# Kernel optimization log

Measured on AMD Instinct MI355X. Metric: run time of the kernel, lower is better.

Reference implementation:

```python
import jax, jax.numpy as jnp
import numpy as np

THRESHOLD = 0.5
SLACK = 3
EPS = 1e-12
B, H, W = 16, 512, 512


def _shift(p, dy, dx, b, h, w):
    # p is zero-padded by 1 on spatial dims; returns neighbor at offset (dy, dx)
    return p[:, 1 + dy:1 + dy + h, 1 + dx:1 + dx + w]


def _thin_sub(img, step):
    # One Zhang-Suen sub-iteration on bool image [B,H,W] (zero boundary, as skimage)
    b, h, w = img.shape
    p = jnp.pad(img.astype(jnp.int32), ((0, 0), (1, 1), (1, 1)))
    # P2..P9 clockwise starting at North
    P2 = _shift(p, -1, 0, b, h, w); P3 = _shift(p, -1, 1, b, h, w)
    P4 = _shift(p, 0, 1, b, h, w);  P5 = _shift(p, 1, 1, b, h, w)
    P6 = _shift(p, 1, 0, b, h, w);  P7 = _shift(p, 1, -1, b, h, w)
    P8 = _shift(p, 0, -1, b, h, w); P9 = _shift(p, -1, -1, b, h, w)
    seq = [P2, P3, P4, P5, P6, P7, P8, P9, P2]
    Bn = P2 + P3 + P4 + P5 + P6 + P7 + P8 + P9          # neighbor count
    A = sum((1 - seq[k]) * seq[k + 1] for k in range(8))  # 0->1 transitions
    cond = (Bn >= 2) & (Bn <= 6) & (A == 1)
    if step == 0:
        cond = cond & (P2 * P4 * P6 == 0) & (P4 * P6 * P8 == 0)
    else:
        cond = cond & (P2 * P4 * P8 == 0) & (P2 * P6 * P8 == 0)
    return img & ~cond


def _skeletonize(img):
    # Iterate Zhang-Suen thinning to convergence (skimage.morphology.skeletonize 2D = Zhang's method)
    def body(state):
        cur, _ = state
        nxt = _thin_sub(_thin_sub(cur, 0), 1)
        return (nxt, jnp.any(nxt != cur))

    out, _ = jax.lax.while_loop(lambda s: s[1], body, (img, jnp.array(True)))
    return out


def _edt_sq(mask):
    # Exact squared Euclidean distance to nearest True pixel, separable 2-pass.
    b, h, w = mask.shape
    BIG = h + w  # larger than any attainable 1D distance
    g = jnp.where(mask, 0, BIG).astype(jnp.int32)  # [B,H,W]

    # pass 1: 1D nearest-True distance along rows (axis=1) via fwd/bwd scans
    def fscan(carry, row):
        d = jnp.minimum(row, carry + 1)
        return d, d

    g_rows = jnp.moveaxis(g, 1, 0)  # [H,B,W]
    init = jnp.full((b, w), BIG, jnp.int32)
    _, fwd = jax.lax.scan(fscan, init, g_rows)
    _, bwd = jax.lax.scan(fscan, init, g_rows[::-1])
    f = jnp.minimum(jnp.minimum(fwd, bwd[::-1]), BIG)  # [H,B,W]
    f2 = jnp.moveaxis(f * f, 0, 1)  # [B,H,W] squared vertical distance

    # pass 2: d2[b,i,j] = min_{j'} f2[b,i,j'] + (j-j')^2 (lower envelope, memory-friendly lax.map)
    js = jnp.arange(w, dtype=jnp.int32)

    def one_col(j):
        off = (js - j) ** 2  # [W]
        return jnp.min(f2 + off[None, None, :], axis=-1)  # [B,H]

    d2 = jax.lax.map(one_col, js)  # [W,B,H]
    return jnp.transpose(d2, (1, 2, 0))  # [B,H,W]


def setup_inputs() -> dict:
    key = jax.random.key(0)
    k1, k2 = jax.random.split(key)
    y_pred = jax.random.uniform(k1, (B, H, W), dtype=jnp.float32)
    y_true = jax.random.uniform(k2, (B, H, W), dtype=jnp.float32)
    return {"y_pred": y_pred, "y_true": y_true}


def reference(y_pred, y_true):
    p = y_pred > THRESHOLD  # greater_is_road=True binarization
    g = y_true > THRESHOLD
    p = _skeletonize(p)
    g = _skeletonize(g)
    d2_gt = _edt_sq(g)   # EDT of ~g == distance to nearest g pixel
    d2_pr = _edt_sq(p)
    s2 = SLACK * SLACK   # dist <= slack  <=>  dist^2 <= slack^2 (integer sq EDT)
    tp_area = d2_gt <= s2
    fp_area = ~tp_area
    fn_area = d2_pr > s2
    ax = (1, 2)
    TP = jnp.sum(tp_area & p, ax).astype(jnp.float32)
    FP = jnp.sum(fp_area & p, ax).astype(jnp.float32)
    FN = jnp.sum(fn_area & g, ax).astype(jnp.float32)
    correctness = TP / (TP + FP + EPS)
    completeness = TP / (TP + FN + EPS)
    quality = TP / (TP + FP + FN + EPS)
    # mean over batch -> [3]: [correctness, completeness, quality]
    return jnp.mean(jnp.stack([correctness, completeness, quality], axis=1), axis=0)
```

## Files before the change

kernel.cpp:

```cpp
#include <hip/hip_runtime.h>
#include <stdint.h>

#define HH 512
#define WW 512
#define WPR 8
#define NWORDS (HH * WPR)
#define NTHREADS 1024
#define WPT (NWORDS / NTHREADS)
#define NB 16

typedef unsigned long long u64;

__device__ __forceinline__ u64 ldw(const u64* M, int r, int c) {
    return (r < 0 || r >= HH || c < 0 || c >= WPR) ? 0ULL : M[r * WPR + c];
}

__device__ __forceinline__ u64 zs_word(const u64* M, int r, int c, int step) {
    u64 nm = ldw(M, r - 1, c - 1), nc = ldw(M, r - 1, c), np = ldw(M, r - 1, c + 1);
    u64 cm = ldw(M, r,     c - 1), cc = ldw(M, r,     c), cp = ldw(M, r,     c + 1);
    u64 sm = ldw(M, r + 1, c - 1), sc = ldw(M, r + 1, c), sp = ldw(M, r + 1, c + 1);

    u64 P2 = nc;
    u64 P3 = (nc >> 1) | (np << 63);
    u64 P4 = (cc >> 1) | (cp << 63);
    u64 P5 = (sc >> 1) | (sp << 63);
    u64 P6 = sc;
    u64 P7 = (sc << 1) | (sm >> 63);
    u64 P8 = (cc << 1) | (cm >> 63);
    u64 P9 = (nc << 1) | (nm >> 63);

    u64 ab = P2 ^ P3;
    u64 s1 = ab ^ P4, c1 = (P2 & P3) | (ab & P4);
    u64 de = P5 ^ P6;
    u64 s2 = de ^ P7, c2 = (P5 & P6) | (de & P7);
    u64 s3 = P8 ^ P9, c3 = P8 & P9;
    u64 gh = s1 ^ s2;
    u64 b0 = gh ^ s3, c4 = (s1 & s2) | (gh & s3);
    u64 ij = c1 ^ c2;
    u64 s4 = ij ^ c3, c5 = (c1 & c2) | (ij & c3);
    u64 b1 = s4 ^ c4, c6 = s4 & c4;
    u64 b2 = c5 ^ c6, b3 = c5 & c6;

    u64 Bge2 = b1 | b2 | b3;
    u64 Ble6 = ~(b3 | (b2 & b1 & b0));

    u64 a1, a2, t;
    t = ~P2 & P3; a1 = t; a2 = 0ULL;
    t = ~P3 & P4; a2 |= a1 & t; a1 |= t;
    t = ~P4 & P5; a2 |= a1 & t; a1 |= t;
    t = ~P5 & P6; a2 |= a1 & t; a1 |= t;
    t = ~P6 & P7; a2 |= a1 & t; a1 |= t;
    t = ~P7 & P8; a2 |= a1 & t; a1 |= t;
    t = ~P8 & P9; a2 |= a1 & t; a1 |= t;
    t = ~P9 & P2; a2 |= a1 & t; a1 |= t;
    u64 Aeq1 = a1 & ~a2;

    u64 sccond;
    if (step == 0) sccond = ~(P2 & P4 & P6) & ~(P4 & P6 & P8);
    else           sccond = ~(P2 & P4 & P8) & ~(P2 & P6 & P8);

    return cc & ~(Bge2 & Ble6 & Aeq1 & sccond);
}

__global__ __launch_bounds__(NTHREADS)
void skel_kernel(const float* __restrict__ y_pred,
                 const float* __restrict__ y_true,
                 u64* __restrict__ skel ,
                 int* __restrict__ cnt ) {
    __shared__ u64 M[NWORDS];
    __shared__ unsigned int Cp[HH + 2];
    __shared__ int s_any[2];

    int bx = blockIdx.x;
    int tid = threadIdx.x;
    int lane = tid & 63;

    if (bx == 0 && tid < 4 * NB) cnt[tid] = 0;

    const float* src = (bx < NB) ? y_pred + (size_t)bx * HH * WW
                                 : y_true + (size_t)(bx - NB) * HH * WW;

    {
        unsigned short* M16 = (unsigned short*)M;
        const float4* s4 = (const float4*)src;
        #pragma unroll
        for (int i = 0; i < 16; ++i) {
            int t = i * NTHREADS + tid;
            float4 a = s4[t * 4 + 0];
            float4 b = s4[t * 4 + 1];
            float4 c = s4[t * 4 + 2];
            float4 d = s4[t * 4 + 3];
            unsigned bits =
                ((unsigned)(a.x > 0.5f) << 0)  | ((unsigned)(a.y > 0.5f) << 1)  |
                ((unsigned)(a.z > 0.5f) << 2)  | ((unsigned)(a.w > 0.5f) << 3)  |
                ((unsigned)(b.x > 0.5f) << 4)  | ((unsigned)(b.y > 0.5f) << 5)  |
                ((unsigned)(b.z > 0.5f) << 6)  | ((unsigned)(b.w > 0.5f) << 7)  |
                ((unsigned)(c.x > 0.5f) << 8)  | ((unsigned)(c.y > 0.5f) << 9)  |
                ((unsigned)(c.z > 0.5f) << 10) | ((unsigned)(c.w > 0.5f) << 11) |
                ((unsigned)(d.x > 0.5f) << 12) | ((unsigned)(d.y > 0.5f) << 13) |
                ((unsigned)(d.z > 0.5f) << 14) | ((unsigned)(d.w > 0.5f) << 15);
            M16[t] = (unsigned short)bits;
        }
    }

    for (int i = tid; i < HH + 2; i += NTHREADS)
        Cp[i] = (i >= 1 && i <= HH) ? 0x1FEu : 0u;
    if (tid < 2) s_any[tid] = 0;

    unsigned dl[WPT];
    #pragma unroll
    for (int k = 0; k < WPT; ++k) dl[k] = 0x1FEu;

    int p = 0;
    for (;;) {
        for (int step = 0; step < 2; ++step) {
            __syncthreads();
            u64 nv[WPT];
            u64 bal[WPT];
            bool anyc = false;
            #pragma unroll
            for (int k = 0; k < WPT; ++k) {
                int wi = k * NTHREADS + tid;
                int r = wi >> 3, c = wi & 7;
                unsigned need = ((Cp[r] | Cp[r + 1] | Cp[r + 2]) >> c) & 7u;
                bool chg = false;
                u64 x = 0;
                if (need) {
                    u64 cur = M[wi];
                    x = zs_word(M, r, c, step);
                    chg = (x != cur);
                }
                nv[k] = x;
                bal[k] = __ballot(chg);
                anyc |= (bal[k] != 0);
            }
            __syncthreads();
            #pragma unroll
            for (int k = 0; k < WPT; ++k) {
                int wi = k * NTHREADS + tid;
                if ((bal[k] >> lane) & 1) M[wi] = nv[k];
                if ((lane & 7) == 0) {
                    unsigned byte = ((unsigned)(bal[k] >> lane) & 0xFFu) << 1;
                    int idx = (wi >> 3) + 1;
                    Cp[idx] = byte | dl[k];
                    dl[k] = byte;
                }
            }
            if (anyc) s_any[p] = 1;
        }
        __syncthreads();
        int done = (s_any[p] == 0);
        if (tid == 0) s_any[p ^ 1] = 0;
        p ^= 1;
        if (done) break;
    }

    u64* dst = skel + (size_t)bx * NWORDS;
    #pragma unroll
    for (int k = 0; k < WPT; ++k) {
        int wi = k * NTHREADS + tid;
        dst[wi] = M[wi];
    }
}

#define STRIPS 8
#define SROWS (HH / STRIPS)
#define SR2 (SROWS + 6)

__device__ __forceinline__ u64 ldws(const u64* M, int r, int c) {
    return (c < 0 || c >= WPR) ? 0ULL : M[r * WPR + c];
}

__device__ __forceinline__ u64 dil3s(const u64* M, int r, int c) {
    u64 cm = ldws(M, r, c - 1), cc = ldws(M, r, c), cp = ldws(M, r, c + 1);
    u64 h = cc
          | (cc >> 1) | (cp << 63)
          | (cc >> 2) | (cp << 62)
          | (cc >> 3) | (cp << 61)
          | (cc << 1) | (cm >> 63)
          | (cc << 2) | (cm >> 62)
          | (cc << 3) | (cm >> 61);
    u64 um = ldws(M, r - 1, c - 1) | ldws(M, r + 1, c - 1) | ldws(M, r - 2, c - 1) | ldws(M, r + 2, c - 1);
    u64 uc = ldws(M, r - 1, c    ) | ldws(M, r + 1, c    ) | ldws(M, r - 2, c    ) | ldws(M, r + 2, c    );
    u64 up = ldws(M, r - 1, c + 1) | ldws(M, r + 1, c + 1) | ldws(M, r - 2, c + 1) | ldws(M, r + 2, c + 1);
    h |= uc
       | (uc >> 1) | (up << 63)
       | (uc >> 2) | (up << 62)
       | (uc << 1) | (um >> 63)
       | (uc << 2) | (um >> 62);
    h |= ldws(M, r - 3, c) | ldws(M, r + 3, c);
    return h;
}

__global__ __launch_bounds__(256)
void count_kernel(const u64* __restrict__ skel, int* __restrict__ cnt) {
    __shared__ u64 P[SR2 * WPR];
    __shared__ u64 G[SR2 * WPR];
    __shared__ int acc[4];

    int b = blockIdx.x / STRIPS;
    int s = blockIdx.x % STRIPS;
    int tid = threadIdx.x;
    int r0 = s * SROWS - 3;

    const u64* sp = skel + (size_t)b * NWORDS;
    const u64* sg = skel + (size_t)(NB + b) * NWORDS;
    for (int i = tid; i < SR2 * WPR; i += 256) {
        int gr = r0 + (i >> 3);
        bool in = (gr >= 0 && gr < HH);
        int gi = gr * WPR + (i & 7);
        P[i] = in ? sp[gi] : 0ULL;
        G[i] = in ? sg[gi] : 0ULL;
    }
    if (tid < 4) acc[tid] = 0;
    __syncthreads();

    int cp = 0, cg = 0, tp = 0, fnh = 0;
    #pragma unroll
    for (int k = 0; k < 2; ++k) {
        int w = k * 256 + tid;
        int r = (w >> 3) + 3, c = w & 7;
        u64 pw = P[r * WPR + c], gw = G[r * WPR + c];
        cp  += __popcll(pw);
        cg  += __popcll(gw);
        tp  += __popcll(pw & dil3s(G, r, c));
        fnh += __popcll(gw & dil3s(P, r, c));
    }
    #pragma unroll
    for (int o = 32; o > 0; o >>= 1) {
        cp  += __shfl_down(cp, o);
        cg  += __shfl_down(cg, o);
        tp  += __shfl_down(tp, o);
        fnh += __shfl_down(fnh, o);
    }
    if ((tid & 63) == 0) {
        atomicAdd(&acc[0], cp);
        atomicAdd(&acc[1], cg);
        atomicAdd(&acc[2], tp);
        atomicAdd(&acc[3], fnh);
    }
    __syncthreads();
    if (tid < 4) atomicAdd(&cnt[b * 4 + tid], acc[tid]);
}

__global__ void ccq_reduce(const int* __restrict__ cnt, float* __restrict__ out) {
    int k = threadIdx.x;
    if (k < 3) {
        float s = 0.0f;
        for (int b = 0; b < NB; ++b) {
            float TP = (float)cnt[b * 4 + 2];
            float FP = (float)(cnt[b * 4 + 0] - cnt[b * 4 + 2]);
            float FN = (float)(cnt[b * 4 + 1] - cnt[b * 4 + 3]);
            float v = (k == 0) ? TP / (TP + FP + 1e-12f)
                    : (k == 1) ? TP / (TP + FN + 1e-12f)
                               : TP / (TP + FP + FN + 1e-12f);
            s += v;
        }
        out[k] = s * (1.0f / NB);
    }
}

extern "C" void kernel_launch(void* const* d_in, const int* in_sizes, int n_in,
                              void* d_out, int out_size, void* d_ws, size_t ws_size,
                              hipStream_t stream) {
    (void)in_sizes; (void)n_in; (void)out_size; (void)ws_size;
    const float* y_pred = (const float*)d_in[0];
    const float* y_true = (const float*)d_in[1];
    float* out = (float*)d_out;

    u64* skel = (u64*)d_ws;
    int* cnt = (int*)((char*)d_ws + (size_t)2 * NB * NWORDS * sizeof(u64));

    hipLaunchKernelGGL(skel_kernel, dim3(2 * NB), dim3(NTHREADS), 0, stream,
                       y_pred, y_true, skel, cnt);
    hipLaunchKernelGGL(count_kernel, dim3(NB * STRIPS), dim3(256), 0, stream,
                       skel, cnt);
    hipLaunchKernelGGL(ccq_reduce, dim3(1), dim3(64), 0, stream, cnt, out);
}
```

Before: 130.1 us.

## Split binarization into a wide pack kernel and double-buffer the thinning state

Moves the float-to-bit thresholding out of the 32-block skeleton kernel into a separate pack kernel that runs across many blocks, so the 32 MB input read uses the whole GPU instead of 32 CUs. The thinning loop now ping-pongs between two shared-memory bitmaps and change maps, with a three-slot convergence flag. This removes one of the two barriers per sub-iteration and the extra per-iteration convergence barrier. The cost is an extra kernel launch, a global round trip of the packed bits, and every word being written each sub-iteration.

```diff
diff --git a/kernel.cpp b/kernel.cpp
--- a/kernel.cpp
+++ b/kernel.cpp
@@ -3,6 +3,7 @@
 
 #define HH 512
 #define WW 512
+#define HW (HH * WW)
 #define WPR 8
 #define NWORDS (HH * WPR)
 #define NTHREADS 1024
@@ -15,9 +16,9 @@
     return (r < 0 || r >= HH || c < 0 || c >= WPR) ? 0ULL : M[r * WPR + c];
 }
 
-__device__ __forceinline__ u64 zs_word(const u64* M, int r, int c, int step) {
+__device__ __forceinline__ u64 zs_word(const u64* M, u64 cc, int r, int c, int step) {
     u64 nm = ldw(M, r - 1, c - 1), nc = ldw(M, r - 1, c), np = ldw(M, r - 1, c + 1);
-    u64 cm = ldw(M, r,     c - 1), cc = ldw(M, r,     c), cp = ldw(M, r,     c + 1);
+    u64 cm = ldw(M, r,     c - 1),                        cp = ldw(M, r,     c + 1);
     u64 sm = ldw(M, r + 1, c - 1), sc = ldw(M, r + 1, c), sp = ldw(M, r + 1, c + 1);
 
     u64 P2 = nc;
@@ -62,104 +63,118 @@
     return cc & ~(Bge2 & Ble6 & Aeq1 & sccond);
 }
 
+__global__ __launch_bounds__(256)
+void pack_kernel(const float* __restrict__ y_pred,
+                 const float* __restrict__ y_true,
+                 u64* __restrict__ bits ,
+                 int* __restrict__ cnt ) {
+    int tid = threadIdx.x;
+    if (blockIdx.x == 0 && tid < 4 * NB) cnt[tid] = 0;
+
+    int t = blockIdx.x * 256 + tid;
+    size_t g0 = (size_t)t * 16;
+    const float* src;
+    size_t off;
+    if (g0 < (size_t)NB * HW) { src = y_pred; off = g0; }
+    else                      { src = y_true; off = g0 - (size_t)NB * HW; }
+    const float4* s4 = (const float4*)(src + off);
+    float4 a = s4[0];
+    float4 b = s4[1];
+    float4 c = s4[2];
+    float4 d = s4[3];
+    unsigned m =
+        ((unsigned)(a.x > 0.5f) << 0)  | ((unsigned)(a.y > 0.5f) << 1)  |
+        ((unsigned)(a.z > 0.5f) << 2)  | ((unsigned)(a.w > 0.5f) << 3)  |
+        ((unsigned)(b.x > 0.5f) << 4)  | ((unsigned)(b.y > 0.5f) << 5)  |
+        ((unsigned)(b.z > 0.5f) << 6)  | ((unsigned)(b.w > 0.5f) << 7)  |
+        ((unsigned)(c.x > 0.5f) << 8)  | ((unsigned)(c.y > 0.5f) << 9)  |
+        ((unsigned)(c.z > 0.5f) << 10) | ((unsigned)(c.w > 0.5f) << 11) |
+        ((unsigned)(d.x > 0.5f) << 12) | ((unsigned)(d.y > 0.5f) << 13) |
+        ((unsigned)(d.z > 0.5f) << 14) | ((unsigned)(d.w > 0.5f) << 15);
+    ((unsigned short*)bits)[t] = (unsigned short)m;
+}
+
 __global__ __launch_bounds__(NTHREADS)
-void skel_kernel(const float* __restrict__ y_pred,
-                 const float* __restrict__ y_true,
-                 u64* __restrict__ skel ,
-                 int* __restrict__ cnt ) {
-    __shared__ u64 M[NWORDS];
-    __shared__ unsigned int Cp[HH + 2];
-    __shared__ int s_any[2];
+void skel_kernel(u64* __restrict__ bits ) {
+    __shared__ u64 Mb[2][NWORDS];
+    __shared__ unsigned int Cpb[2][HH + 2];
+    __shared__ int s_any[3];
 
     int bx = blockIdx.x;
     int tid = threadIdx.x;
     int lane = tid & 63;
 
-    if (bx == 0 && tid < 4 * NB) cnt[tid] = 0;
-
-    const float* src = (bx < NB) ? y_pred + (size_t)bx * HH * WW
-                                 : y_true + (size_t)(bx - NB) * HH * WW;
+    u64* gm = bits + (size_t)bx * NWORDS;
 
     {
-        unsigned short* M16 = (unsigned short*)M;
-        const float4* s4 = (const float4*)src;
+        const ulonglong2* s2 = (const ulonglong2*)gm;
+        ulonglong2* m2 = (ulonglong2*)Mb[0];
         #pragma unroll
-        for (int i = 0; i < 16; ++i) {
-            int t = i * NTHREADS + tid;
-            float4 a = s4[t * 4 + 0];
-            float4 b = s4[t * 4 + 1];
-            float4 c = s4[t * 4 + 2];
-            float4 d = s4[t * 4 + 3];
-            unsigned bits =
-                ((unsigned)(a.x > 0.5f) << 0)  | ((unsigned)(a.y > 0.5f) << 1)  |
-                ((unsigned)(a.z > 0.5f) << 2)  | ((unsigned)(a.w > 0.5f) << 3)  |
-                ((unsigned)(b.x > 0.5f) << 4)  | ((unsigned)(b.y > 0.5f) << 5)  |
-                ((unsigned)(b.z > 0.5f) << 6)  | ((unsigned)(b.w > 0.5f) << 7)  |
-                ((unsigned)(c.x > 0.5f) << 8)  | ((unsigned)(c.y > 0.5f) << 9)  |
-                ((unsigned)(c.z > 0.5f) << 10) | ((unsigned)(c.w > 0.5f) << 11) |
-                ((unsigned)(d.x > 0.5f) << 12) | ((unsigned)(d.y > 0.5f) << 13) |
-                ((unsigned)(d.z > 0.5f) << 14) | ((unsigned)(d.w > 0.5f) << 15);
-            M16[t] = (unsigned short)bits;
-        }
-    }
-
-    for (int i = tid; i < HH + 2; i += NTHREADS)
-        Cp[i] = (i >= 1 && i <= HH) ? 0x1FEu : 0u;
-    if (tid < 2) s_any[tid] = 0;
+        for (int k = 0; k < 2; ++k) {
+            int i = k * NTHREADS + tid;
+            m2[i] = s2[i];
+        }
+    }
+
+    for (int i = tid; i < HH + 2; i += NTHREADS) {
+        Cpb[0][i] = (i >= 1 && i <= HH) ? 0x1FEu : 0u;
+        Cpb[1][i] = 0u;
+    }
+    if (tid < 3) s_any[tid] = 0;
 
     unsigned dl[WPT];
     #pragma unroll
     for (int k = 0; k < WPT; ++k) dl[k] = 0x1FEu;
 
-    int p = 0;
+    int it = 0;
+    bool done = false;
     for (;;) {
         for (int step = 0; step < 2; ++step) {
             __syncthreads();
-            u64 nv[WPT];
-            u64 bal[WPT];
+            if (step == 0 && it > 0) {
+                if (s_any[(it + 2) % 3] == 0) { done = true; break; }
+            }
+            const u64* Ms = Mb[step];
+            u64* Md = Mb[step ^ 1];
+            const unsigned* CpS = Cpb[step];
+            unsigned* CpD = Cpb[step ^ 1];
             bool anyc = false;
             #pragma unroll
             for (int k = 0; k < WPT; ++k) {
                 int wi = k * NTHREADS + tid;
                 int r = wi >> 3, c = wi & 7;
-                unsigned need = ((Cp[r] | Cp[r + 1] | Cp[r + 2]) >> c) & 7u;
+                unsigned need = ((CpS[r] | CpS[r + 1] | CpS[r + 2]) >> c) & 7u;
+                u64 cur = Ms[wi];
+                u64 x = cur;
                 bool chg = false;
-                u64 x = 0;
                 if (need) {
-                    u64 cur = M[wi];
-                    x = zs_word(M, r, c, step);
+                    x = zs_word(Ms, cur, r, c, step);
                     chg = (x != cur);
                 }
-                nv[k] = x;
-                bal[k] = __ballot(chg);
-                anyc |= (bal[k] != 0);
-            }
-            __syncthreads();
-            #pragma unroll
-            for (int k = 0; k < WPT; ++k) {
-                int wi = k * NTHREADS + tid;
-                if ((bal[k] >> lane) & 1) M[wi] = nv[k];
+                Md[wi] = x;
+                u64 bal = __ballot(chg);
+                anyc |= (bal != 0);
                 if ((lane & 7) == 0) {
-                    unsigned byte = ((unsigned)(bal[k] >> lane) & 0xFFu) << 1;
-                    int idx = (wi >> 3) + 1;
-                    Cp[idx] = byte | dl[k];
+                    unsigned byte = ((unsigned)(bal >> lane) & 0xFFu) << 1;
+                    CpD[(wi >> 3) + 1] = byte | dl[k];
                     dl[k] = byte;
                 }
             }
-            if (anyc) s_any[p] = 1;
-        }
-        __syncthreads();
-        int done = (s_any[p] == 0);
-        if (tid == 0) s_any[p ^ 1] = 0;
-        p ^= 1;
+            if (anyc) s_any[it % 3] = 1;
+            if (step == 1 && tid == 0) s_any[(it + 1) % 3] = 0;
+        }
         if (done) break;
-    }
-
-    u64* dst = skel + (size_t)bx * NWORDS;
-    #pragma unroll
-    for (int k = 0; k < WPT; ++k) {
-        int wi = k * NTHREADS + tid;
-        dst[wi] = M[wi];
+        ++it;
+    }
+
+    {
+        ulonglong2* d2 = (ulonglong2*)gm;
+        const ulonglong2* m2 = (const ulonglong2*)Mb[0];
+        #pragma unroll
+        for (int k = 0; k < 2; ++k) {
+            int i = k * NTHREADS + tid;
+            d2[i] = m2[i];
+        }
     }
 }
 
@@ -268,12 +283,13 @@
     const float* y_true = (const float*)d_in[1];
     float* out = (float*)d_out;
 
-    u64* skel = (u64*)d_ws;
+    u64* bits = (u64*)d_ws;
     int* cnt = (int*)((char*)d_ws + (size_t)2 * NB * NWORDS * sizeof(u64));
 
-    hipLaunchKernelGGL(skel_kernel, dim3(2 * NB), dim3(NTHREADS), 0, stream,
-                       y_pred, y_true, skel, cnt);
+    hipLaunchKernelGGL(pack_kernel, dim3(2 * NB * HW / 16 / 256), dim3(256), 0, stream,
+                       y_pred, y_true, bits, cnt);
+    hipLaunchKernelGGL(skel_kernel, dim3(2 * NB), dim3(NTHREADS), 0, stream, bits);
     hipLaunchKernelGGL(count_kernel, dim3(NB * STRIPS), dim3(256), 0, stream,
-                       skel, cnt);
+                       bits, cnt);
     hipLaunchKernelGGL(ccq_reduce, dim3(1), dim3(64), 0, stream, cnt, out);
 }
```

Result: faster. 115.7 us (-11.1%).
